# Performance work log

Measured on AMD Instinct MI355X. Metric: run time of the kernel, lower is better.

Reference implementation:

```python
import jax, jax.numpy as jnp
import numpy as np

IN, H, HC, HQ, OUT = 7, 64, 32, 16, 3  # input, shared hidden, cell hidden, head hidden, per-task out
B, S = 256, 2048


def setup_inputs() -> dict:
    key = jax.random.key(0)
    ks = iter(jax.random.split(key, 40))
    def p(shape, scale=0.1):
        return jax.random.normal(next(ks), shape, dtype=jnp.float32) * scale
    d = {}
    d['x'] = jax.random.normal(next(ks), (B, S, IN), dtype=jnp.float32)
    # shared LSTM (torch gate order i,f,g,o)
    d['W_ih_s'] = p((4 * H, IN)); d['W_hh_s'] = p((4 * H, H))
    d['b_ih_s'] = p((4 * H,));    d['b_hh_s'] = p((4 * H,))
    # attitude cell: input = [shared_h(64), x(7)]
    d['W_ih_a'] = p((4 * HC, H + IN)); d['W_hh_a'] = p((4 * HC, HC))
    d['b_ih_a'] = p((4 * HC,));        d['b_hh_a'] = p((4 * HC,))
    # velocity cell: input = [shared_h(64), delta_att(3), x(7)]
    d['W_ih_v'] = p((4 * HC, H + OUT + IN)); d['W_hh_v'] = p((4 * HC, HC))
    d['b_ih_v'] = p((4 * HC,));              d['b_hh_v'] = p((4 * HC,))
    # position cell: input = [shared_h(64), delta_vel(3)]
    d['W_ih_p'] = p((4 * HC, H + OUT)); d['W_hh_p'] = p((4 * HC, HC))
    d['b_ih_p'] = p((4 * HC,));         d['b_hh_p'] = p((4 * HC,))
    # per-task readout MLPs (dropout is identity in eval mode)
    d['Wa1'] = p((HQ, HC)); d['ba1'] = p((HQ,)); d['Wa2'] = p((OUT, HQ)); d['ba2'] = p((OUT,))
    d['Wv1'] = p((HQ, HC)); d['bv1'] = p((HQ,)); d['Wv2'] = p((OUT, HQ)); d['bv2'] = p((OUT,))
    d['Wp1'] = p((HQ, HC)); d['bp1'] = p((HQ,)); d['Wp2'] = p((OUT, HQ)); d['bp2'] = p((OUT,))
    return d


def lstm_cell(x, h, c, Wih, Whh, bih, bhh):
    z = x @ Wih.T + h @ Whh.T + bih + bhh
    i, f, g, o = jnp.split(z, 4, axis=-1)
    c = jax.nn.sigmoid(f) * c + jax.nn.sigmoid(i) * jnp.tanh(g)
    h = jax.nn.sigmoid(o) * jnp.tanh(c)
    return h, c


def mlp(h, W1, b1, W2, b2):
    return jax.nn.relu(h @ W1.T + b1) @ W2.T + b2


def reference(x, W_ih_s, W_hh_s, b_ih_s, b_hh_s,
              W_ih_a, W_hh_a, b_ih_a, b_hh_a,
              W_ih_v, W_hh_v, b_ih_v, b_hh_v,
              W_ih_p, W_hh_p, b_ih_p, b_hh_p,
              Wa1, ba1, Wa2, ba2, Wv1, bv1, Wv2, bv2, Wp1, bp1, Wp2, bp2):
    b = x.shape[0]
    z = lambda n: jnp.zeros((b, n), x.dtype)
    carry0 = (z(H), z(H), z(HC), z(HC), z(HC), z(HC), z(HC), z(HC))

    def step(carry, xt):
        hs, cs, ha, ca, hv, cv, hp, cp = carry
        hs, cs = lstm_cell(xt, hs, cs, W_ih_s, W_hh_s, b_ih_s, b_hh_s)
        ha, ca = lstm_cell(jnp.concatenate([hs, xt], -1), ha, ca,
                           W_ih_a, W_hh_a, b_ih_a, b_hh_a)
        d_att = mlp(ha, Wa1, ba1, Wa2, ba2)
        hv, cv = lstm_cell(jnp.concatenate([hs, jax.lax.stop_gradient(d_att), xt], -1),
                           hv, cv, W_ih_v, W_hh_v, b_ih_v, b_hh_v)
        d_vel = mlp(hv, Wv1, bv1, Wv2, bv2)
        hp, cp = lstm_cell(jnp.concatenate([hs, jax.lax.stop_gradient(d_vel)], -1),
                           hp, cp, W_ih_p, W_hh_p, b_ih_p, b_hh_p)
        d_pos = mlp(hp, Wp1, bp1, Wp2, bp2)
        out = jnp.concatenate([d_att, d_vel, d_pos], -1)  # [B, 9]
        return (hs, cs, ha, ca, hv, cv, hp, cp), out

    _, ys = jax.lax.scan(step, carry0, jnp.swapaxes(x, 0, 1))  # [S, B, 9]
    return jnp.swapaxes(ys, 0, 1)  # [B, S, 9]
```

## Files before the change

### kernel.cpp

```cpp
#include <hip/hip_runtime.h>

typedef unsigned int u32;

#define NIN 7
#define NB 256
#define NS 2048

__device__ __forceinline__ float fastrcp(float x){ return __builtin_amdgcn_rcpf(x); }
__device__ __forceinline__ float sigf(float x){ return fastrcp(1.f + __expf(-x)); }
__device__ __forceinline__ float tanhf_(float x){ return 1.f - 2.f*fastrcp(1.f + __expf(2.f*x)); }

__device__ __forceinline__ u32 pkh(float a, float b){
  unsigned short ua = __builtin_bit_cast(unsigned short, (_Float16)a);
  unsigned short ub = __builtin_bit_cast(unsigned short, (_Float16)b);
  return (u32)ua | ((u32)ub << 16);
}

template<int J>
__device__ __forceinline__ float rlf(float v){
  return __uint_as_float((unsigned)__builtin_amdgcn_readlane((int)__float_as_uint(v), J));
}
__device__ __forceinline__ float rlfv(float v, int j){
  return __uint_as_float((unsigned)__builtin_amdgcn_readlane((int)__float_as_uint(v), j));
}

__device__ __forceinline__ float mxl(float acc, u32 wp, float a){
  asm("v_fma_mix_f32 %0, %1, %2, %3 op_sel_hi:[1,0,0]"
      : "=v"(acc) : "v"(wp), "s"(a), "0"(acc));
  return acc;
}
__device__ __forceinline__ float mxh(float acc, u32 wp, float a){
  asm("v_fma_mix_f32 %0, %1, %2, %3 op_sel:[1,0,0] op_sel_hi:[1,0,0]"
      : "=v"(acc) : "v"(wp), "s"(a), "0"(acc));
  return acc;
}
__device__ __forceinline__ float mxlv(float acc, u32 wp, float a){
  asm("v_fma_mix_f32 %0, %1, %2, %3 op_sel_hi:[1,0,0]"
      : "=v"(acc) : "v"(wp), "v"(a), "0"(acc));
  return acc;
}
__device__ __forceinline__ float mxhv(float acc, u32 wp, float a){
  asm("v_fma_mix_f32 %0, %1, %2, %3 op_sel:[1,0,0] op_sel_hi:[1,0,0]"
      : "=v"(acc) : "v"(wp), "v"(a), "0"(acc));
  return acc;
}

__device__ __forceinline__ float gate4(float zi, float zf, float zg, float zo, float& c){
  c = sigf(zf)*c + sigf(zi)*tanhf_(zg);
  return sigf(zo)*tanhf_(c);
}

#define XD(a0, a1, KB, v0, v1) { \
  a0 = mxlv(a0, w[(KB)+0], (v0).x); a1 = mxhv(a1, w[(KB)+0], (v0).y); \
  a0 = mxlv(a0, w[(KB)+1], (v0).z); a1 = mxhv(a1, w[(KB)+1], (v0).w); \
  a0 = mxlv(a0, w[(KB)+2], (v1).x); a1 = mxhv(a1, w[(KB)+2], (v1).y); \
  a0 = mxlv(a0, w[(KB)+3], (v1).z); a1 = mxhv(a1, w[(KB)+3], (v1).w); }

#define MX2(a0, a1, s0, s1, KA, KS, SRC) { _Pragma("unroll") \
  for (int k_ = 0; k_ < 32; k_++){ \
    float e0_ = rlfv(SRC, 2*k_), e1_ = rlfv(SRC, 2*k_+1); \
    a0 = mxl(a0, w[(KA)+k_], e0_); a1 = mxh(a1, w[(KA)+k_], e1_); \
    s0 = mxl(s0, w[(KS)+k_], e0_); s1 = mxh(s1, w[(KS)+k_], e1_); } }

#define MX1(a0, a1, KA, SRC) { _Pragma("unroll") \
  for (int k_ = 0; k_ < 32; k_++){ \
    float e0_ = rlfv(SRC, 2*k_), e1_ = rlfv(SRC, 2*k_+1); \
    a0 = mxl(a0, w[(KA)+k_], e0_); a1 = mxh(a1, w[(KA)+k_], e1_); } }

#define MXH16(z0, z1, KB, SRC) { _Pragma("unroll") \
  for (int k_ = 0; k_ < 16; k_++){ \
    float e0_ = rlfv(SRC, 2*k_), e1_ = rlfv(SRC, 2*k_+1); \
    z0 = mxl(z0, w[(KB)+k_], e0_); z1 = mxh(z1, w[(KB)+k_], e1_); } }

#define MLPX(HS_, M1B, B1V, M2B, B2V, dres) { \
  float q0_ = (B1V), q1_ = 0.f; \
  _Pragma("unroll") \
  for (int j_ = 0; j_ < 16; j_++){ \
    float e0_ = rlfv(HS_, 2*j_), e1_ = rlfv(HS_, 2*j_+1); \
    q0_ = mxl(q0_, w[(M1B)+j_], e0_); q1_ = mxh(q1_, w[(M1B)+j_], e1_); } \
  float qq_ = fmaxf(q0_+q1_, 0.f); \
  float f0_ = (B2V), f1_ = 0.f; \
  _Pragma("unroll") \
  for (int j_ = 0; j_ < 8; j_++){ \
    float e0_ = rlfv(qq_, 2*j_), e1_ = rlfv(qq_, 2*j_+1); \
    f0_ = mxl(f0_, w[(M2B)+j_], e0_); f1_ = mxh(f1_, w[(M2B)+j_], e1_); } \
  dres = f0_ + f1_; }

__global__ __launch_bounds__(512, 1) void mtinn_kernel(
    const float* __restrict__ x,
    const float* wihs, const float* whhs, const float* bihs, const float* bhhs,
    const float* wiha, const float* whha, const float* biha, const float* bhha,
    const float* wihv, const float* whhv, const float* bihv, const float* bhhv,
    const float* wihp, const float* whhp, const float* bihp, const float* bhhp,
    const float* wa1, const float* ba1, const float* wa2, const float* ba2,
    const float* wv1, const float* bv1, const float* wv2, const float* bv2,
    const float* wp1, const float* bp1, const float* wp2, const float* bp2,
    float* __restrict__ out)
{
  __shared__ __align__(16) float ZS[2][256];
  __shared__ __align__(16) float ZC[3][128];
  __shared__ __align__(16) float HS[64];
  __shared__ __align__(16) float HA[32], HV[32];
  __shared__ __align__(16) float HPb[2][32];
  __shared__ __align__(16) float XL[4][8];

  const int tid  = threadIdx.x;
  const int wave = tid >> 6, lane = tid & 63, l = lane & 31;
  const int b    = blockIdx.x;
  const float* xb = x + (size_t)b * NS * NIN;

  const bool isWin = (wave != 0 && wave != 4);
  const int  wc    = (wave==1||wave==7) ? 0 : (wave==2||wave==5) ? 1 : 2;
  const int  wrb   = (wave <= 3) ? 64 : 0;
  const bool isSh  = (wave==1 || wave==2 || wave==6 || wave==7);
  const int  qoff  = (wave==1) ? 0 : (wave==2) ? 64 : (wave==6) ? 128 : 192;
  const int  mi = lane & 15, mm = lane % 3;

  u32 w[88];
#pragma unroll
  for (int i = 0; i < 88; i++) w[i] = 0u;
  float b1a=0.f,b2a=0.f,b1v=0.f,b2v=0.f,b1p=0.f,b2p=0.f;

  if (isWin){
    const float* wih = (wc==0) ? wiha : (wc==1) ? wihv : wihp;
    const float* whh = (wc==0) ? whha : (wc==1) ? whhv : whhp;
    const float* bi  = (wc==0) ? biha : (wc==1) ? bihv : bihp;
    const float* bh  = (wc==0) ? bhha : (wc==1) ? bhhv : bhhp;
    const int L = (wc==0) ? 71 : (wc==1) ? 74 : 67;
    const int r = wrb + lane;
#pragma unroll
    for (int k=0;k<16;k++) w[k] = pkh(whh[r*32+2*k], whh[r*32+2*k+1]);
#pragma unroll
    for (int k=0;k<32;k++) w[16+k] = pkh(wih[r*L+2*k], wih[r*L+2*k+1]);
    const float bsum = bi[r] + bh[r];
    if (wc==0){
      w[48]=pkh(wih[r*L+64],wih[r*L+65]); w[49]=pkh(wih[r*L+66],wih[r*L+67]);
      w[50]=pkh(wih[r*L+68],wih[r*L+69]); w[51]=pkh(wih[r*L+70], bsum);
    } else if (wc==1){
      w[48]=pkh(wih[r*L+67],wih[r*L+68]); w[49]=pkh(wih[r*L+69],wih[r*L+70]);
      w[50]=pkh(wih[r*L+71],wih[r*L+72]); w[51]=pkh(wih[r*L+73], bsum);
    } else {
      w[51]=pkh(0.f, bsum);
    }
  }
  if (isSh){
    const int r = qoff + lane;
#pragma unroll
    for (int k=0;k<32;k++) w[52+k] = pkh(whhs[r*64+2*k], whhs[r*64+2*k+1]);
    w[84]=pkh(wihs[r*7+0],wihs[r*7+1]); w[85]=pkh(wihs[r*7+2],wihs[r*7+3]);
    w[86]=pkh(wihs[r*7+4],wihs[r*7+5]); w[87]=pkh(wihs[r*7+6], bihs[r]+bhhs[r]);
  }
  if (wave == 0){
#pragma unroll
    for (int k=0;k<16;k++){
      w[k]    = pkh(wa1[mi*32+2*k], wa1[mi*32+2*k+1]);
      w[16+k] = pkh(wv1[mi*32+2*k], wv1[mi*32+2*k+1]);
    }
#pragma unroll
    for (int k=0;k<8;k++){
      w[48+k] = pkh(wa2[mm*16+2*k], wa2[mm*16+2*k+1]);
      w[56+k] = pkh(wv2[mm*16+2*k], wv2[mm*16+2*k+1]);
    }
#pragma unroll
    for (int g=0; g<4; g++){
      int rr = g*32 + l;
      w[72+2*g]   = pkh(wihv[rr*74+64], wihv[rr*74+65]);
      w[72+2*g+1] = pkh(wihv[rr*74+66], 0.f);
      w[80+2*g]   = pkh(wihp[rr*67+64], wihp[rr*67+65]);
      w[80+2*g+1] = pkh(wihp[rr*67+66], 0.f);
    }
    b1a=ba1[mi]; b2a=ba2[mm]; b1v=bv1[mi]; b2v=bv2[mm];
  }
  if (wave == 4){
#pragma unroll
    for (int k=0;k<16;k++) w[k] = pkh(wp1[mi*32+2*k], wp1[mi*32+2*k+1]);
#pragma unroll
    for (int k=0;k<8;k++)  w[16+k] = pkh(wp2[mm*16+2*k], wp2[mm*16+2*k+1]);
    b1p=bp1[mi]; b2p=bp2[mm];
  }

  if (tid < 32) HA[tid]=0.f;
  else if (tid < 64)  HV[tid-32]=0.f;
  else if (tid < 96)  HPb[0][tid-64]=0.f;
  else if (tid < 128) HPb[1][tid-96]=0.f;
  if (tid < 8){
    XL[0][tid] = (tid<7) ? xb[tid]         : 1.f;
    XL[1][tid] = (tid<7) ? xb[NIN+tid]     : 1.f;
    XL[2][tid] = (tid<7) ? xb[2*NIN+tid]   : 1.f;
    XL[3][tid] = 1.f;
  }
  __syncthreads();

  if (isSh){
    const float4* X0 = (const float4*)XL[0];
    float4 xa = X0[0], xb4 = X0[1];
    float s0=0.f, s1=0.f; XD(s0,s1,84,xa,xb4);
    ZS[0][qoff + lane] = s0 + s1;
  }
  __syncthreads();

  float c_s = 0.f;
  float c_a = 0.f, c_v = 0.f, c_p = 0.f;
  float zpart = 0.f;

  if (isWin){
    float zi_=ZS[0][lane], zf_=ZS[0][64+lane], zg_=ZS[0][128+lane], zo_=ZS[0][192+lane];
    float hsv = gate4(zi_,zf_,zg_,zo_, c_s);
    const float4* X0 = (const float4*)XL[0];
    float4 xa = X0[0], xb4 = X0[1];
    float a0=0.f, a1=0.f; XD(a0,a1,48,xa,xb4);
    if (isSh){
      const float4* X1 = (const float4*)XL[1];
      float4 xc = X1[0], xd = X1[1];
      float s0=0.f, s1=0.f; XD(s0,s1,84,xc,xd);
      MX2(a0,a1,s0,s1,16,52,hsv);
      ZS[1][qoff + lane] = s0 + s1;
    } else {
      MX1(a0,a1,16,hsv);
    }
    zpart = a0 + a1;
  }
  __syncthreads();

#pragma unroll 1
  for (int t = 0; t < NS; t++){
    float xpre = 0.f;
    if (wave == 0){
      if (lane < 7){
        const int tf = (t+3 < NS) ? t+3 : NS-1;
        xpre = xb[(size_t)tf*NIN + lane];
      }
    } else if (wave == 4){
      if (t > 0){
        float hp_ = HPb[(t^1)&1][l];
        float dP; MLPX(hp_, 0, b1p, 16, b2p, dP);
        if (lane < 3) out[((size_t)b*NS + (t-1))*9 + 6 + lane] = dP;
      }
    } else {
      const float* Hsrc = (wc==0) ? HA : (wc==1) ? HV : HPb[(t^1)&1];
      float h = Hsrc[l];
      if (wave == 7){
        const float* Zsrc = ZS[(t+1)&1];
        float zi_=Zsrc[lane], zf_=Zsrc[64+lane], zg_=Zsrc[128+lane], zo_=Zsrc[192+lane];
        float hsv2 = gate4(zi_,zf_,zg_,zo_, c_s);
        HS[lane] = hsv2;
      }
      float z0 = zpart, z1 = 0.f;
      MXH16(z0,z1,0,h);
      ZC[wc][wrb + lane] = z0 + z1;
    }
    __syncthreads();

    if (wave == 0){
      __builtin_amdgcn_s_setprio(1);
      float zai=ZC[0][l], zaf=ZC[0][32+l], zag=ZC[0][64+l], zao=ZC[0][96+l];
      float zvi=ZC[1][l], zvf=ZC[1][32+l], zvg=ZC[1][64+l], zvo=ZC[1][96+l];
      float zpi=ZC[2][l], zpf=ZC[2][32+l], zpg=ZC[2][64+l], zpo=ZC[2][96+l];
      float* ob = out + ((size_t)b*NS + t)*9;
      float ha = gate4(zai,zaf,zag,zao, c_a);
      if (lane < 32) HA[lane] = ha;
      float dA; MLPX(ha, 0, b1a, 48, b2a, dA);
      if (lane < 3) ob[lane] = dA;
      float dx=rlf<0>(dA), dy=rlf<1>(dA), dz=rlf<2>(dA);
      zvi = mxl(zvi, w[72], dx); zvi = mxh(zvi, w[72], dy); zvi = mxl(zvi, w[73], dz);
      zvf = mxl(zvf, w[74], dx); zvf = mxh(zvf, w[74], dy); zvf = mxl(zvf, w[75], dz);
      zvg = mxl(zvg, w[76], dx); zvg = mxh(zvg, w[76], dy); zvg = mxl(zvg, w[77], dz);
      zvo = mxl(zvo, w[78], dx); zvo = mxh(zvo, w[78], dy); zvo = mxl(zvo, w[79], dz);
      float hv = gate4(zvi,zvf,zvg,zvo, c_v);
      if (lane < 32) HV[lane] = hv;
      float dV; MLPX(hv, 16, b1v, 56, b2v, dV);
      if (lane < 3) ob[3+lane] = dV;
      dx=rlf<0>(dV); dy=rlf<1>(dV); dz=rlf<2>(dV);
      zpi = mxl(zpi, w[80], dx); zpi = mxh(zpi, w[80], dy); zpi = mxl(zpi, w[81], dz);
      zpf = mxl(zpf, w[82], dx); zpf = mxh(zpf, w[82], dy); zpf = mxl(zpf, w[83], dz);
      zpg = mxl(zpg, w[84], dx); zpg = mxh(zpg, w[84], dy); zpg = mxl(zpg, w[85], dz);
      zpo = mxl(zpo, w[86], dx); zpo = mxh(zpo, w[86], dy); zpo = mxl(zpo, w[87], dz);
      float hp_ = gate4(zpi,zpf,zpg,zpo, c_p);
      if (lane < 32) HPb[t&1][lane] = hp_;
      __builtin_amdgcn_s_setprio(0);
      if (lane < 7) XL[(t+3)&3][lane] = xpre;
    } else if (isWin){
      float hsv = HS[lane];
      const float4* X1 = (const float4*)XL[(t+1)&3];
      float4 xa = X1[0], xb4 = X1[1];
      float a0=0.f, a1=0.f; XD(a0,a1,48,xa,xb4);
      if (isSh){
        const float4* X2 = (const float4*)XL[(t+2)&3];
        float4 xc = X2[0], xd = X2[1];
        float s0=0.f, s1=0.f; XD(s0,s1,84,xc,xd);
        MX2(a0,a1,s0,s1,16,52,hsv);
        ZS[t&1][qoff + lane] = s0 + s1;
      } else {
        MX1(a0,a1,16,hsv);
      }
      zpart = a0 + a1;
    }
    __syncthreads();
  }

  if (wave == 4){
    float hp_ = HPb[(NS-1)&1][l];
    float dP; MLPX(hp_, 0, b1p, 16, b2p, dP);
    if (lane < 3) out[((size_t)b*NS + (NS-1))*9 + 6 + lane] = dP;
  }
}

extern "C" void kernel_launch(void* const* d_in, const int* in_sizes, int n_in,
                              void* d_out, int out_size, void* d_ws, size_t ws_size,
                              hipStream_t stream) {
  (void)in_sizes; (void)n_in; (void)d_ws; (void)ws_size; (void)out_size;
  const float* X    = (const float*)d_in[0];
  const float* Wihs = (const float*)d_in[1];
  const float* Whhs = (const float*)d_in[2];
  const float* Bihs = (const float*)d_in[3];
  const float* Bhhs = (const float*)d_in[4];
  const float* Wiha = (const float*)d_in[5];
  const float* Whha = (const float*)d_in[6];
  const float* Biha = (const float*)d_in[7];
  const float* Bhha = (const float*)d_in[8];
  const float* Wihv = (const float*)d_in[9];
  const float* Whhv = (const float*)d_in[10];
  const float* Bihv = (const float*)d_in[11];
  const float* Bhhv = (const float*)d_in[12];
  const float* Wihp = (const float*)d_in[13];
  const float* Whhp = (const float*)d_in[14];
  const float* Bihp = (const float*)d_in[15];
  const float* Bhhp = (const float*)d_in[16];
  const float* Wa1  = (const float*)d_in[17];
  const float* Ba1  = (const float*)d_in[18];
  const float* Wa2  = (const float*)d_in[19];
  const float* Ba2  = (const float*)d_in[20];
  const float* Wv1  = (const float*)d_in[21];
  const float* Bv1  = (const float*)d_in[22];
  const float* Wv2  = (const float*)d_in[23];
  const float* Bv2  = (const float*)d_in[24];
  const float* Wp1  = (const float*)d_in[25];
  const float* Bp1  = (const float*)d_in[26];
  const float* Wp2  = (const float*)d_in[27];
  const float* Bp2  = (const float*)d_in[28];
  float* OUTP = (float*)d_out;

  mtinn_kernel<<<dim3(NB), dim3(512), 0, stream>>>(
      X, Wihs, Whhs, Bihs, Bhhs,
      Wiha, Whha, Biha, Bhha,
      Wihv, Whhv, Bihv, Bhhv,
      Wihp, Whhp, Bihp, Bhhp,
      Wa1, Ba1, Wa2, Ba2, Wv1, Bv1, Wv2, Bv2, Wp1, Bp1, Wp2, Bp2,
      OUTP);
}
```

Baseline: 2.871 ms.

## Broadcast hidden states via LDS float4 loads instead of readlane chains

Replaces the per-element v_readlane broadcasts of hidden states in the shared and cell matvecs with uniform float4 loads from LDS, using the vector-operand fma_mix variants. The shared-LSTM gate computation moves from wave 7 to wave 4 (which also runs it once in the prologue to keep its cell state in step), lightening the cell-matvec waves. Launch bounds are changed to request two blocks per CU, which constrains register allocation. The aim is to cut the serial SALU readlane traffic on the recurrence critical path, at the cost of more LDS reads and possible register pressure or spills.

```diff
diff --git a/kernel.cpp b/kernel.cpp
--- a/kernel.cpp
+++ b/kernel.cpp
@@ -56,6 +56,26 @@
   a0 = mxlv(a0, w[(KB)+2], (v1).x); a1 = mxhv(a1, w[(KB)+2], (v1).y); \
   a0 = mxlv(a0, w[(KB)+3], (v1).z); a1 = mxhv(a1, w[(KB)+3], (v1).w); }
 
+#define LMX2(a0, a1, s0, s1, KA, KS, H4) { _Pragma("unroll") \
+  for (int c_ = 0; c_ < 16; c_++){ \
+    float4 h_ = (H4)[c_]; \
+    a0 = mxlv(a0, w[(KA)+2*c_],   h_.x); a1 = mxhv(a1, w[(KA)+2*c_],   h_.y); \
+    a0 = mxlv(a0, w[(KA)+2*c_+1], h_.z); a1 = mxhv(a1, w[(KA)+2*c_+1], h_.w); \
+    s0 = mxlv(s0, w[(KS)+2*c_],   h_.x); s1 = mxhv(s1, w[(KS)+2*c_],   h_.y); \
+    s0 = mxlv(s0, w[(KS)+2*c_+1], h_.z); s1 = mxhv(s1, w[(KS)+2*c_+1], h_.w); } }
+
+#define LMX1(a0, a1, KA, H4) { _Pragma("unroll") \
+  for (int c_ = 0; c_ < 16; c_++){ \
+    float4 h_ = (H4)[c_]; \
+    a0 = mxlv(a0, w[(KA)+2*c_],   h_.x); a1 = mxhv(a1, w[(KA)+2*c_],   h_.y); \
+    a0 = mxlv(a0, w[(KA)+2*c_+1], h_.z); a1 = mxhv(a1, w[(KA)+2*c_+1], h_.w); } }
+
+#define LMXH(z0, z1, KB, H4) { _Pragma("unroll") \
+  for (int c_ = 0; c_ < 8; c_++){ \
+    float4 h_ = (H4)[c_]; \
+    z0 = mxlv(z0, w[(KB)+2*c_],   h_.x); z1 = mxhv(z1, w[(KB)+2*c_],   h_.y); \
+    z0 = mxlv(z0, w[(KB)+2*c_+1], h_.z); z1 = mxhv(z1, w[(KB)+2*c_+1], h_.w); } }
+
 #define MX2(a0, a1, s0, s1, KA, KS, SRC) { _Pragma("unroll") \
   for (int k_ = 0; k_ < 32; k_++){ \
     float e0_ = rlfv(SRC, 2*k_), e1_ = rlfv(SRC, 2*k_+1); \
@@ -66,11 +86,6 @@
   for (int k_ = 0; k_ < 32; k_++){ \
     float e0_ = rlfv(SRC, 2*k_), e1_ = rlfv(SRC, 2*k_+1); \
     a0 = mxl(a0, w[(KA)+k_], e0_); a1 = mxh(a1, w[(KA)+k_], e1_); } }
-
-#define MXH16(z0, z1, KB, SRC) { _Pragma("unroll") \
-  for (int k_ = 0; k_ < 16; k_++){ \
-    float e0_ = rlfv(SRC, 2*k_), e1_ = rlfv(SRC, 2*k_+1); \
-    z0 = mxl(z0, w[(KB)+k_], e0_); z1 = mxh(z1, w[(KB)+k_], e1_); } }
 
 #define MLPX(HS_, M1B, B1V, M2B, B2V, dres) { \
   float q0_ = (B1V), q1_ = 0.f; \
@@ -86,7 +101,7 @@
     f0_ = mxl(f0_, w[(M2B)+j_], e0_); f1_ = mxh(f1_, w[(M2B)+j_], e1_); } \
   dres = f0_ + f1_; }
 
-__global__ __launch_bounds__(512, 1) void mtinn_kernel(
+__global__ __launch_bounds__(512, 2) void mtinn_kernel(
     const float* __restrict__ x,
     const float* wihs, const float* whhs, const float* bihs, const float* bhhs,
     const float* wiha, const float* whha, const float* biha, const float* bhha,
@@ -219,6 +234,9 @@
       MX1(a0,a1,16,hsv);
     }
     zpart = a0 + a1;
+  } else if (wave == 4){
+    float zi_=ZS[0][lane], zf_=ZS[0][64+lane], zg_=ZS[0][128+lane], zo_=ZS[0][192+lane];
+    gate4(zi_,zf_,zg_,zo_, c_s);
   }
   __syncthreads();
 
@@ -231,22 +249,19 @@
         xpre = xb[(size_t)tf*NIN + lane];
       }
     } else if (wave == 4){
+      const float* Zsrc = ZS[(t+1)&1];
+      float zi_=Zsrc[lane], zf_=Zsrc[64+lane], zg_=Zsrc[128+lane], zo_=Zsrc[192+lane];
+      float hsv2 = gate4(zi_,zf_,zg_,zo_, c_s);
+      HS[lane] = hsv2;
       if (t > 0){
         float hp_ = HPb[(t^1)&1][l];
         float dP; MLPX(hp_, 0, b1p, 16, b2p, dP);
         if (lane < 3) out[((size_t)b*NS + (t-1))*9 + 6 + lane] = dP;
       }
     } else {
-      const float* Hsrc = (wc==0) ? HA : (wc==1) ? HV : HPb[(t^1)&1];
-      float h = Hsrc[l];
-      if (wave == 7){
-        const float* Zsrc = ZS[(t+1)&1];
-        float zi_=Zsrc[lane], zf_=Zsrc[64+lane], zg_=Zsrc[128+lane], zo_=Zsrc[192+lane];
-        float hsv2 = gate4(zi_,zf_,zg_,zo_, c_s);
-        HS[lane] = hsv2;
-      }
+      const float4* H4 = (const float4*)((wc==0) ? HA : (wc==1) ? HV : HPb[(t^1)&1]);
       float z0 = zpart, z1 = 0.f;
-      MXH16(z0,z1,0,h);
+      LMXH(z0,z1,0,H4);
       ZC[wc][wrb + lane] = z0 + z1;
     }
     __syncthreads();
@@ -280,7 +295,7 @@
       __builtin_amdgcn_s_setprio(0);
       if (lane < 7) XL[(t+3)&3][lane] = xpre;
     } else if (isWin){
-      float hsv = HS[lane];
+      const float4* H4 = (const float4*)HS;
       const float4* X1 = (const float4*)XL[(t+1)&3];
       float4 xa = X1[0], xb4 = X1[1];
       float a0=0.f, a1=0.f; XD(a0,a1,48,xa,xb4);
@@ -288,10 +303,10 @@
         const float4* X2 = (const float4*)XL[(t+2)&3];
         float4 xc = X2[0], xd = X2[1];
         float s0=0.f, s1=0.f; XD(s0,s1,84,xc,xd);
-        MX2(a0,a1,s0,s1,16,52,hsv);
+        LMX2(a0,a1,s0,s1,16,52,H4);
         ZS[t&1][qoff + lane] = s0 + s1;
       } else {
-        MX1(a0,a1,16,hsv);
+        LMX1(a0,a1,16,H4);
       }
       zpart = a0 + a1;
     }
```

Result: no change. 2.817 ms (-1.9%).
